# Kernel tuning notes

Measured on AMD Instinct MI355X. Metric: run time of the kernel, lower is better.

The kernel has to match this reference:

```python
import jax, jax.numpy as jnp
import numpy as np

TEMPERATURE = 0.5


def setup_inputs() -> dict:
    key = jax.random.key(0)
    k1, k2 = jax.random.split(key)
    emb = jax.random.normal(k1, (16384, 128), dtype=jnp.float32)
    emb = emb / jnp.linalg.norm(emb, axis=1, keepdims=True)  # L2-normalized, per docstring
    labels = jax.random.randint(k2, (16384,), 0, 64, dtype=jnp.int64)
    return {"embeddings": emb, "partition_labels": labels}


def reference(embeddings, partition_labels):
    n = embeddings.shape[0]
    # [N, N] similarity matrix, scaled by temperature
    sim = jnp.matmul(embeddings, embeddings.T) / TEMPERATURE
    exp_sim = jnp.exp(sim)
    eye = jnp.eye(n, dtype=bool)
    pos_mask = (partition_labels[None, :] == partition_labels[:, None]) & ~eye
    # numerator: sum of exp over positives; denominator: sum over all k != i
    pos_sum = jnp.sum(jnp.where(pos_mask, exp_sim, 0.0), axis=1)
    all_sum = jnp.sum(jnp.where(~eye, exp_sim, 0.0), axis=1)
    valid = jnp.any(pos_mask, axis=1)
    loss_i = -(jnp.log(pos_sum) - jnp.log(all_sum))
    n_valid = jnp.sum(valid)
    total = jnp.sum(jnp.where(valid, loss_i, 0.0))
    return jnp.where(n_valid > 0, total / n_valid, 0.0)
```

## Files before the change

kernel.cpp:

```cpp
#include <hip/hip_runtime.h>

#define N_EMB 16384
#define DIM 128
#define NSPLIT 8
#define CPS (N_EMB / NSPLIT)
#define BN 128
#define NCT (CPS / BN)
#define NLAB 64

typedef __bf16 bf16x8 __attribute__((ext_vector_type(8)));
typedef float f32x4 __attribute__((ext_vector_type(4)));
typedef unsigned short us8 __attribute__((ext_vector_type(8)));
typedef unsigned int u32;

#define SCALE 2.8853900817779268f
#define LN2 0.6931471805599453f

__device__ inline float fast_exp2(float x) {
#if __has_builtin(__builtin_amdgcn_exp2f)
  return __builtin_amdgcn_exp2f(x);
#else
  return exp2f(x);
#endif
}
__device__ inline float fast_log2(float x) {
#if __has_builtin(__builtin_amdgcn_logf)
  return __builtin_amdgcn_logf(x);
#else
  return log2f(x);
#endif
}

__device__ inline unsigned short f2bf(float f) {
  unsigned int u = __float_as_uint(f);
  u += 0x7fffu + ((u >> 16) & 1u);
  return (unsigned short)(u >> 16);
}

__device__ inline void gll16(const unsigned short* g, unsigned short* l) {
  __builtin_amdgcn_global_load_lds(
      (const __attribute__((address_space(1))) u32*)g,
      (__attribute__((address_space(3))) u32*)l, 16, 0, 0);
}

__global__ __launch_bounds__(1024) void perm_kernel(
    const int* __restrict__ labels, int* __restrict__ perm,
    int* __restrict__ gstart) {
  __shared__ int whist[16][NLAB];
  __shared__ int htot[NLAB];
  const int tid = threadIdx.x;
  const int w = tid >> 6, lane = tid & 63;
  whist[w][lane] = 0;
  __syncthreads();
  const int base_i = w * 1024;
  int mylab[16];
#pragma unroll
  for (int k = 0; k < 16; ++k) {
    int lab = labels[base_i + k * 64 + lane];
    mylab[k] = lab;
    atomicAdd(&whist[w][lab], 1);
  }
  __syncthreads();
  if (tid < NLAB) {
    int s = 0;
#pragma unroll
    for (int ww = 0; ww < 16; ++ww) {
      int t = whist[ww][tid];
      whist[ww][tid] = s;
      s += t;
    }
    htot[tid] = s;
  }
  __syncthreads();
  if (tid == 0) {
    int s = 0;
    for (int l = 0; l < NLAB; ++l) {
      int t = htot[l];
      gstart[l] = s;
      htot[l] = s;
      s += t;
    }
    gstart[NLAB] = s;
  }
  __syncthreads();
  whist[w][lane] += htot[lane];
  __syncthreads();
#pragma unroll
  for (int k = 0; k < 16; ++k) {
    int lab = mylab[k];
    int pos = atomicAdd(&whist[w][lab], 1);
    perm[pos] = base_i + k * 64 + lane;
  }
}

__global__ __launch_bounds__(256) void preconv(
    const float* __restrict__ emb, const int* __restrict__ perm,
    unsigned short* __restrict__ eraw) {
  const int tid = threadIdx.x;
  const int tile = blockIdx.x >> 2;
  const int part = blockIdx.x & 3;
  const size_t base = (size_t)tile * (128 * DIM);
#pragma unroll
  for (int i = 0; i < 2; ++i) {
    int G = part * 512 + i * 256 + tid;
    int col16 = G & 15;
    int qd = (G >> 4) & 3;
    int ks = (G >> 6) & 3;
    int tc = G >> 8;
    int srow = perm[tile * 128 + tc * 16 + col16];
    const float* p = emb + (size_t)srow * DIM + ks * 32 + qd * 8;
    float4 a = *reinterpret_cast<const float4*>(p);
    float4 b = *reinterpret_cast<const float4*>(p + 4);
    us8 g;
    g[0] = f2bf(a.x); g[1] = f2bf(a.y); g[2] = f2bf(a.z); g[3] = f2bf(a.w);
    g[4] = f2bf(b.x); g[5] = f2bf(b.y); g[6] = f2bf(b.z); g[7] = f2bf(b.w);
    *reinterpret_cast<us8*>(eraw + base + (size_t)G * 8) = g;
  }
}

__device__ inline bf16x8 load_scaled(const unsigned short* p) {
  us8 v = *reinterpret_cast<const us8*>(p);
  us8 s;
#pragma unroll
  for (int j = 0; j < 8; ++j)
    s[j] = f2bf(__uint_as_float((u32)v[j] << 16) * SCALE);
  return *reinterpret_cast<bf16x8*>(&s);
}

__device__ inline void loadB(bf16x8* dst,
                             const unsigned short* __restrict__ eraw, int T,
                             int lane) {
  const unsigned short* p =
      eraw + (size_t)(T >> 3) * (128 * DIM) + ((T & 7) * 4) * 512 + lane * 8;
#pragma unroll
  for (int ks = 0; ks < 4; ++ks)
    dst[ks] = *reinterpret_cast<const bf16x8*>(p + ks * 512);
}

__global__ __launch_bounds__(128) void cl_fused(
    const unsigned short* __restrict__ eraw, const int* __restrict__ gstart,
    float* __restrict__ ws_all, float* __restrict__ ws_pos,
    float* __restrict__ ws_diag) {
  __shared__ unsigned short lds[BN * DIM];
  const int tid = threadIdx.x;
  const int lane = tid & 63;
  const int w = tid >> 6;
  const int col16 = lane & 15;
  const int quad = lane >> 4;
  const int cs = blockIdx.y;

  if (cs < NSPLIT) {
    const int r0 = blockIdx.x * 128;

    bf16x8 afrag[4][4];
#pragma unroll
    for (int tr = 0; tr < 4; ++tr) {
      const int T = (r0 >> 4) + w * 4 + tr;
      const unsigned short* p = eraw + (size_t)(T >> 3) * (128 * DIM) +
                                ((T & 7) * 4) * 512 + lane * 8;
#pragma unroll
      for (int ks = 0; ks < 4; ++ks) afrag[tr][ks] = load_scaled(p + ks * 512);
    }

    float all_p[16];
#pragma unroll
    for (int t = 0; t < 16; ++t) all_p[t] = 0.f;

    for (int ct = 0; ct < NCT; ++ct) {
      const int c0 = cs * CPS + ct * BN;
      __syncthreads();
      {
        const unsigned short* g = eraw + (size_t)(c0 >> 7) * (128 * DIM);
#pragma unroll
        for (int i = 0; i < 16; ++i) {
          int chunk = i * 2 + w;
          gll16(g + chunk * 512 + lane * 8, lds + chunk * 512);
        }
      }
      __syncthreads();

#pragma unroll
      for (int tc = 0; tc < 8; ++tc) {
        bf16x8 bfr[4];
#pragma unroll
        for (int ks = 0; ks < 4; ++ks)
          bfr[ks] = *reinterpret_cast<const bf16x8*>(lds + (tc * 4 + ks) * 512 +
                                                     lane * 8);
#pragma unroll
        for (int tr = 0; tr < 4; ++tr) {
          f32x4 acc = {0.f, 0.f, 0.f, 0.f};
#pragma unroll
          for (int ks = 0; ks < 4; ++ks)
            acc = __builtin_amdgcn_mfma_f32_16x16x32_bf16(afrag[tr][ks],
                                                          bfr[ks], acc, 0, 0,
                                                          0);
#pragma unroll
          for (int r = 0; r < 4; ++r) all_p[tr * 4 + r] += fast_exp2(acc[r]);
        }
      }
    }

#pragma unroll
    for (int t = 0; t < 16; ++t) {
      float a = all_p[t];
#pragma unroll
      for (int m = 8; m >= 1; m >>= 1) a += __shfl_xor(a, m, 64);
      if (col16 == 0) {
        int row_g = r0 + w * 64 + (t >> 2) * 16 + quad * 4 + (t & 3);
        ws_all[cs * N_EMB + row_g] = a;
      }
    }
  } else {
    const int l = blockIdx.x >> 1;
    const int sub = blockIdx.x & 1;
    const int gs = gstart[l], ge = gstart[l + 1];
    const int t0 = gs >> 4;
    const int t1 = (ge + 15) >> 4;

    for (int ta = t0 + sub * 2 + w; ta < t1; ta += 4) {
      bf16x8 af[4];
      const unsigned short* pa = eraw + (size_t)(ta >> 3) * (128 * DIM) +
                                 ((ta & 7) * 4) * 512 + lane * 8;
#pragma unroll
      for (int ks = 0; ks < 4; ++ks) af[ks] = load_scaled(pa + ks * 512);
      const int grow = ta * 16 + quad * 4;
      float posr[4] = {0.f, 0.f, 0.f, 0.f};

      for (int tb = t0; tb < t1; ++tb) {
        bf16x8 bfr[4];
        loadB(bfr, eraw, tb, lane);
        f32x4 acc = {0.f, 0.f, 0.f, 0.f};
#pragma unroll
        for (int ks = 0; ks < 4; ++ks)
          acc = __builtin_amdgcn_mfma_f32_16x16x32_bf16(af[ks], bfr[ks], acc,
                                                        0, 0, 0);
        const int gcol = tb * 16 + col16;
        const bool colin = (gcol >= gs) && (gcol < ge);
#pragma unroll
        for (int r = 0; r < 4; ++r) {
          float e = fast_exp2(acc[r]);
          const int gr = grow + r;
          if (gcol == gr) {
            if (colin) ws_diag[gr] = e;
          } else if (colin) {
            posr[r] += e;
          }
        }
      }

#pragma unroll
      for (int r = 0; r < 4; ++r) {
        float p = posr[r];
#pragma unroll
        for (int m = 8; m >= 1; m >>= 1) p += __shfl_xor(p, m, 64);
        const int gr = grow + r;
        if (col16 == 0 && gr >= gs && gr < ge) ws_pos[gr] = p;
      }
    }
  }
}

__global__ __launch_bounds__(1024) void fin(const float* __restrict__ ws_all,
                                            const float* __restrict__ ws_pos,
                                            const float* __restrict__ ws_diag,
                                            float* __restrict__ out) {
  __shared__ float s_t[1024];
  __shared__ int s_c[1024];
  const int tid = threadIdx.x;
  float tot = 0.f;
  int cnt = 0;
  for (int row = tid; row < N_EMB; row += 1024) {
    float a = 0.f;
#pragma unroll
    for (int s = 0; s < NSPLIT; ++s) a += ws_all[s * N_EMB + row];
    a -= ws_diag[row];
    const float p = ws_pos[row];
    if (p > 0.f) {
      tot += fast_log2(a) - fast_log2(p);
      cnt++;
    }
  }
  s_t[tid] = tot;
  s_c[tid] = cnt;
  __syncthreads();
  for (int s = 512; s > 0; s >>= 1) {
    if (tid < s) {
      s_t[tid] += s_t[tid + s];
      s_c[tid] += s_c[tid + s];
    }
    __syncthreads();
  }
  if (tid == 0)
    out[0] = (s_c[0] > 0) ? (s_t[0] * LN2 / (float)s_c[0]) : 0.f;
}

extern "C" void kernel_launch(void* const* d_in, const int* in_sizes, int n_in,
                              void* d_out, int out_size, void* d_ws,
                              size_t ws_size, hipStream_t stream) {
  const float* emb = (const float*)d_in[0];
  const int* labels = (const int*)d_in[1];

  unsigned short* eraw = (unsigned short*)d_ws;
  float* ws_all = (float*)(eraw + (size_t)N_EMB * DIM);
  float* ws_pos = ws_all + NSPLIT * N_EMB;
  float* ws_diag = ws_pos + N_EMB;
  int* perm = (int*)(ws_diag + N_EMB);
  int* gstart = perm + N_EMB;

  perm_kernel<<<1, 1024, 0, stream>>>(labels, perm, gstart);
  preconv<<<512, 256, 0, stream>>>(emb, perm, eraw);
  cl_fused<<<dim3(128, NSPLIT + 1), 128, 0, stream>>>(eraw, gstart, ws_all,
                                                      ws_pos, ws_diag);
  fin<<<1, 1024, 0, stream>>>(ws_all, ws_pos, ws_diag, (float*)d_out);
}
```

Baseline: 188.8 us.

## Fold positive-pair pass into main blocks using sorted labels and diagonal masking

Removes the separate grid row of positive-sum blocks, which had an irregular per-label workload. Column-split 0 blocks now run a second LDS-tiled pass over the column tiles that cover their row range's label groups, selecting positives by comparing sorted labels. The diagonal is zeroed inline, so the diag workspace disappears, and ws_all is written row-major so fin can read it with float4 loads. The trade-off is that cs=0 blocks carry extra tail work, which may unbalance the grid, and the positive pass recomputes whole 128-column tiles rather than only the exact group range.

New measurement: 173.9 us. -7.9%, faster.

```diff
diff --git a/kernel.cpp b/kernel.cpp
--- a/kernel.cpp
+++ b/kernel.cpp
@@ -45,7 +45,7 @@
 
 __global__ __launch_bounds__(1024) void perm_kernel(
     const int* __restrict__ labels, int* __restrict__ perm,
-    int* __restrict__ gstart) {
+    int* __restrict__ gstart, int* __restrict__ labs) {
   __shared__ int whist[16][NLAB];
   __shared__ int htot[NLAB];
   const int tid = threadIdx.x;
@@ -90,6 +90,7 @@
     int lab = mylab[k];
     int pos = atomicAdd(&whist[w][lab], 1);
     perm[pos] = base_i + k * 64 + lane;
+    labs[pos] = lab;
   }
 }
 
@@ -127,142 +128,155 @@
   return *reinterpret_cast<bf16x8*>(&s);
 }
 
-__device__ inline void loadB(bf16x8* dst,
-                             const unsigned short* __restrict__ eraw, int T,
-                             int lane) {
-  const unsigned short* p =
-      eraw + (size_t)(T >> 3) * (128 * DIM) + ((T & 7) * 4) * 512 + lane * 8;
-#pragma unroll
-  for (int ks = 0; ks < 4; ++ks)
-    dst[ks] = *reinterpret_cast<const bf16x8*>(p + ks * 512);
-}
-
-__global__ __launch_bounds__(128) void cl_fused(
-    const unsigned short* __restrict__ eraw, const int* __restrict__ gstart,
-    float* __restrict__ ws_all, float* __restrict__ ws_pos,
-    float* __restrict__ ws_diag) {
+__global__ __launch_bounds__(128) void cl_main(
+    const unsigned short* __restrict__ eraw, const int* __restrict__ labs,
+    const int* __restrict__ gstart, float* __restrict__ ws_all,
+    float* __restrict__ ws_pos) {
   __shared__ unsigned short lds[BN * DIM];
   const int tid = threadIdx.x;
   const int lane = tid & 63;
   const int w = tid >> 6;
   const int col16 = lane & 15;
   const int quad = lane >> 4;
+  const int r0 = blockIdx.x * 128;
   const int cs = blockIdx.y;
 
-  if (cs < NSPLIT) {
-    const int r0 = blockIdx.x * 128;
-
-    bf16x8 afrag[4][4];
-#pragma unroll
-    for (int tr = 0; tr < 4; ++tr) {
-      const int T = (r0 >> 4) + w * 4 + tr;
-      const unsigned short* p = eraw + (size_t)(T >> 3) * (128 * DIM) +
-                                ((T & 7) * 4) * 512 + lane * 8;
-#pragma unroll
-      for (int ks = 0; ks < 4; ++ks) afrag[tr][ks] = load_scaled(p + ks * 512);
-    }
-
-    float all_p[16];
-#pragma unroll
-    for (int t = 0; t < 16; ++t) all_p[t] = 0.f;
-
-    for (int ct = 0; ct < NCT; ++ct) {
-      const int c0 = cs * CPS + ct * BN;
-      __syncthreads();
-      {
-        const unsigned short* g = eraw + (size_t)(c0 >> 7) * (128 * DIM);
-#pragma unroll
-        for (int i = 0; i < 16; ++i) {
-          int chunk = i * 2 + w;
-          gll16(g + chunk * 512 + lane * 8, lds + chunk * 512);
+  bf16x8 afrag[4][4];
+#pragma unroll
+  for (int tr = 0; tr < 4; ++tr) {
+    const int T = (r0 >> 4) + w * 4 + tr;
+    const unsigned short* p = eraw + (size_t)(T >> 3) * (128 * DIM) +
+                              ((T & 7) * 4) * 512 + lane * 8;
+#pragma unroll
+    for (int ks = 0; ks < 4; ++ks) afrag[tr][ks] = load_scaled(p + ks * 512);
+  }
+
+  float all_p[16];
+#pragma unroll
+  for (int t = 0; t < 16; ++t) all_p[t] = 0.f;
+
+  for (int ct = 0; ct < NCT; ++ct) {
+    const int c0 = cs * CPS + ct * BN;
+    __syncthreads();
+    {
+      const unsigned short* g = eraw + (size_t)(c0 >> 7) * (128 * DIM);
+#pragma unroll
+      for (int i = 0; i < 16; ++i) {
+        int chunk = i * 2 + w;
+        gll16(g + chunk * 512 + lane * 8, lds + chunk * 512);
+      }
+    }
+    __syncthreads();
+
+#pragma unroll
+    for (int tc = 0; tc < 8; ++tc) {
+      bf16x8 bfr[4];
+#pragma unroll
+      for (int ks = 0; ks < 4; ++ks)
+        bfr[ks] = *reinterpret_cast<const bf16x8*>(lds + (tc * 4 + ks) * 512 +
+                                                   lane * 8);
+#pragma unroll
+      for (int tr = 0; tr < 4; ++tr) {
+        f32x4 acc = {0.f, 0.f, 0.f, 0.f};
+#pragma unroll
+        for (int ks = 0; ks < 4; ++ks)
+          acc = __builtin_amdgcn_mfma_f32_16x16x32_bf16(afrag[tr][ks], bfr[ks],
+                                                        acc, 0, 0, 0);
+        const bool diag = (c0 + tc * 16) == (r0 + w * 64 + tr * 16);
+#pragma unroll
+        for (int r = 0; r < 4; ++r) {
+          float e = fast_exp2(acc[r]);
+          if (diag && (quad * 4 + r) == col16) e = 0.f;
+          all_p[tr * 4 + r] += e;
         }
       }
-      __syncthreads();
-
-#pragma unroll
-      for (int tc = 0; tc < 8; ++tc) {
-        bf16x8 bfr[4];
+    }
+  }
+
+#pragma unroll
+  for (int t = 0; t < 16; ++t) {
+    float a = all_p[t];
+#pragma unroll
+    for (int m = 8; m >= 1; m >>= 1) a += __shfl_xor(a, m, 64);
+    if (col16 == 0) {
+      int row_g = r0 + w * 64 + (t >> 2) * 16 + quad * 4 + (t & 3);
+      ws_all[(size_t)row_g * NSPLIT + cs] = a;
+    }
+  }
+
+  if (cs != 0) return;
+
+  int l0 = 0, l1 = 0;
+  for (int l = 0; l < NLAB; ++l) {
+    int gv = gstart[l];
+    if (gv <= r0) l0 = l;
+    if (gv <= r0 + 127) l1 = l;
+  }
+  const int wlo = gstart[l0];
+  const int whi = gstart[l1 + 1];
+  const int t_lo = wlo >> 7;
+  const int t_hi = (whi + 127) >> 7;
+  int labi[16];
+  float pos_p[16];
+#pragma unroll
+  for (int t = 0; t < 16; ++t) {
+    labi[t] = labs[r0 + w * 64 + (t >> 2) * 16 + quad * 4 + (t & 3)];
+    pos_p[t] = 0.f;
+  }
+
+  for (int ct = t_lo; ct < t_hi; ++ct) {
+    const int c0 = ct * BN;
+    __syncthreads();
+    {
+      const unsigned short* g = eraw + (size_t)ct * (128 * DIM);
+#pragma unroll
+      for (int i = 0; i < 16; ++i) {
+        int chunk = i * 2 + w;
+        gll16(g + chunk * 512 + lane * 8, lds + chunk * 512);
+      }
+    }
+    __syncthreads();
+
+#pragma unroll
+    for (int tc = 0; tc < 8; ++tc) {
+      bf16x8 bfr[4];
+#pragma unroll
+      for (int ks = 0; ks < 4; ++ks)
+        bfr[ks] = *reinterpret_cast<const bf16x8*>(lds + (tc * 4 + ks) * 512 +
+                                                   lane * 8);
+      const int labj = labs[c0 + tc * 16 + col16];
+#pragma unroll
+      for (int tr = 0; tr < 4; ++tr) {
+        f32x4 acc = {0.f, 0.f, 0.f, 0.f};
 #pragma unroll
         for (int ks = 0; ks < 4; ++ks)
-          bfr[ks] = *reinterpret_cast<const bf16x8*>(lds + (tc * 4 + ks) * 512 +
-                                                     lane * 8);
-#pragma unroll
-        for (int tr = 0; tr < 4; ++tr) {
-          f32x4 acc = {0.f, 0.f, 0.f, 0.f};
-#pragma unroll
-          for (int ks = 0; ks < 4; ++ks)
-            acc = __builtin_amdgcn_mfma_f32_16x16x32_bf16(afrag[tr][ks],
-                                                          bfr[ks], acc, 0, 0,
-                                                          0);
-#pragma unroll
-          for (int r = 0; r < 4; ++r) all_p[tr * 4 + r] += fast_exp2(acc[r]);
+          acc = __builtin_amdgcn_mfma_f32_16x16x32_bf16(afrag[tr][ks], bfr[ks],
+                                                        acc, 0, 0, 0);
+        const bool diag = (c0 + tc * 16) == (r0 + w * 64 + tr * 16);
+#pragma unroll
+        for (int r = 0; r < 4; ++r) {
+          float e = fast_exp2(acc[r]);
+          if (diag && (quad * 4 + r) == col16) e = 0.f;
+          pos_p[tr * 4 + r] += (labi[tr * 4 + r] == labj) ? e : 0.f;
         }
       }
     }
-
-#pragma unroll
-    for (int t = 0; t < 16; ++t) {
-      float a = all_p[t];
-#pragma unroll
-      for (int m = 8; m >= 1; m >>= 1) a += __shfl_xor(a, m, 64);
-      if (col16 == 0) {
-        int row_g = r0 + w * 64 + (t >> 2) * 16 + quad * 4 + (t & 3);
-        ws_all[cs * N_EMB + row_g] = a;
-      }
-    }
-  } else {
-    const int l = blockIdx.x >> 1;
-    const int sub = blockIdx.x & 1;
-    const int gs = gstart[l], ge = gstart[l + 1];
-    const int t0 = gs >> 4;
-    const int t1 = (ge + 15) >> 4;
-
-    for (int ta = t0 + sub * 2 + w; ta < t1; ta += 4) {
-      bf16x8 af[4];
-      const unsigned short* pa = eraw + (size_t)(ta >> 3) * (128 * DIM) +
-                                 ((ta & 7) * 4) * 512 + lane * 8;
-#pragma unroll
-      for (int ks = 0; ks < 4; ++ks) af[ks] = load_scaled(pa + ks * 512);
-      const int grow = ta * 16 + quad * 4;
-      float posr[4] = {0.f, 0.f, 0.f, 0.f};
-
-      for (int tb = t0; tb < t1; ++tb) {
-        bf16x8 bfr[4];
-        loadB(bfr, eraw, tb, lane);
-        f32x4 acc = {0.f, 0.f, 0.f, 0.f};
-#pragma unroll
-        for (int ks = 0; ks < 4; ++ks)
-          acc = __builtin_amdgcn_mfma_f32_16x16x32_bf16(af[ks], bfr[ks], acc,
-                                                        0, 0, 0);
-        const int gcol = tb * 16 + col16;
-        const bool colin = (gcol >= gs) && (gcol < ge);
-#pragma unroll
-        for (int r = 0; r < 4; ++r) {
-          float e = fast_exp2(acc[r]);
-          const int gr = grow + r;
-          if (gcol == gr) {
-            if (colin) ws_diag[gr] = e;
-          } else if (colin) {
-            posr[r] += e;
-          }
-        }
-      }
-
-#pragma unroll
-      for (int r = 0; r < 4; ++r) {
-        float p = posr[r];
-#pragma unroll
-        for (int m = 8; m >= 1; m >>= 1) p += __shfl_xor(p, m, 64);
-        const int gr = grow + r;
-        if (col16 == 0 && gr >= gs && gr < ge) ws_pos[gr] = p;
-      }
+  }
+
+#pragma unroll
+  for (int t = 0; t < 16; ++t) {
+    float p = pos_p[t];
+#pragma unroll
+    for (int m = 8; m >= 1; m >>= 1) p += __shfl_xor(p, m, 64);
+    if (col16 == 0) {
+      int row_g = r0 + w * 64 + (t >> 2) * 16 + quad * 4 + (t & 3);
+      ws_pos[row_g] = p;
     }
   }
 }
 
 __global__ __launch_bounds__(1024) void fin(const float* __restrict__ ws_all,
                                             const float* __restrict__ ws_pos,
-                                            const float* __restrict__ ws_diag,
                                             float* __restrict__ out) {
   __shared__ float s_t[1024];
   __shared__ int s_c[1024];
@@ -270,10 +284,14 @@
   float tot = 0.f;
   int cnt = 0;
   for (int row = tid; row < N_EMB; row += 1024) {
+    const float4* pa =
+        reinterpret_cast<const float4*>(ws_all + (size_t)row * NSPLIT);
     float a = 0.f;
 #pragma unroll
-    for (int s = 0; s < NSPLIT; ++s) a += ws_all[s * N_EMB + row];
-    a -= ws_diag[row];
+    for (int q = 0; q < NSPLIT / 4; ++q) {
+      float4 va = pa[q];
+      a += va.x + va.y + va.z + va.w;
+    }
     const float p = ws_pos[row];
     if (p > 0.f) {
       tot += fast_log2(a) - fast_log2(p);
@@ -302,14 +320,14 @@
 
   unsigned short* eraw = (unsigned short*)d_ws;
   float* ws_all = (float*)(eraw + (size_t)N_EMB * DIM);
-  float* ws_pos = ws_all + NSPLIT * N_EMB;
-  float* ws_diag = ws_pos + N_EMB;
-  int* perm = (int*)(ws_diag + N_EMB);
+  float* ws_pos = ws_all + (size_t)N_EMB * NSPLIT;
+  int* perm = (int*)(ws_pos + N_EMB);
   int* gstart = perm + N_EMB;
-
-  perm_kernel<<<1, 1024, 0, stream>>>(labels, perm, gstart);
+  int* labs = gstart + 72;
+
+  perm_kernel<<<1, 1024, 0, stream>>>(labels, perm, gstart, labs);
   preconv<<<512, 256, 0, stream>>>(emb, perm, eraw);
-  cl_fused<<<dim3(128, NSPLIT + 1), 128, 0, stream>>>(eraw, gstart, ws_all,
-                                                      ws_pos, ws_diag);
-  fin<<<1, 1024, 0, stream>>>(ws_all, ws_pos, ws_diag, (float*)d_out);
-}
+  cl_main<<<dim3(128, NSPLIT), 128, 0, stream>>>(eraw, labs, gstart, ws_all,
+                                                 ws_pos);
+  fin<<<1, 1024, 0, stream>>>(ws_all, ws_pos, (float*)d_out);
+}
```
